# Optimization experiments

Measured on AMD Instinct MI355X. Metric: run time of the kernel, lower is better.

## Reference

```python
import jax, jax.numpy as jnp
import numpy as np

# Model hyperparameters (hardcoded in GarNetClassificationModel.__init__)
N_BLOCKS, N_AGG, N_FILT, N_PROP = 11, 4, 32, 20
B, V, F_IN = 128, 1024, 10
D_GEX = 2 * F_IN                                   # after GlobalExchange concat
D_UPD = N_FILT + N_AGG * 2 * (N_PROP + N_AGG) + N_AGG  # 32 + 192 + 4 = 228
BN_EPS = 1e-3                                      # keras BatchNormalization default


def setup_inputs() -> dict:
    key = jax.random.key(0)
    ks = iter(jax.random.split(key, 32))
    n = lambda shape, s=0.1: jax.random.normal(next(ks), shape, jnp.float32) * s
    return dict(
        x=jax.random.normal(next(ks), (B, V, F_IN), jnp.float32),
        bn0_gamma=jnp.ones((D_GEX,), jnp.float32),
        bn0_beta=jnp.zeros((D_GEX,), jnp.float32),
        bn0_mean=n((D_GEX,)),
        bn0_var=jax.random.uniform(next(ks), (D_GEX,), jnp.float32, 0.5, 1.5),
        W_in=n((D_GEX, N_FILT), 0.3),
        b_in=jnp.zeros((N_FILT,), jnp.float32),
        W_flr=n((N_BLOCKS, N_FILT, N_PROP), 0.2),
        b_flr=jnp.zeros((N_BLOCKS, N_PROP), jnp.float32),
        W_s=n((N_BLOCKS, N_FILT, N_AGG), 0.2),
        b_s=jnp.zeros((N_BLOCKS, N_AGG), jnp.float32),
        W_out=n((N_BLOCKS, D_UPD, N_FILT), 0.1),
        b_out=jnp.zeros((N_BLOCKS, N_FILT), jnp.float32),
        bn_gamma=jnp.ones((N_BLOCKS, N_FILT), jnp.float32),
        bn_beta=jnp.zeros((N_BLOCKS, N_FILT), jnp.float32),
        bn_mean=n((N_BLOCKS, N_FILT)),
        bn_var=jax.random.uniform(next(ks), (N_BLOCKS, N_FILT), jnp.float32, 0.5, 1.5),
        W_o0=n((N_BLOCKS * N_FILT, 48), 0.1),
        b_o0=jnp.zeros((48,), jnp.float32),
        W_o1=n((48, 3), 0.2),
        b_o1=jnp.zeros((3,), jnp.float32),
    )


def _bn(x, g, b, m, v):
    # inference-mode BatchNormalization over last axis
    return (x - m) * (g * jax.lax.rsqrt(v + BN_EPS)) + b


def reference(x, bn0_gamma, bn0_beta, bn0_mean, bn0_var, W_in, b_in,
              W_flr, b_flr, W_s, b_s, W_out, b_out,
              bn_gamma, bn_beta, bn_mean, bn_var,
              W_o0, b_o0, W_o1, b_o1):
    # GlobalExchange: concat per-event mean over vertices to each vertex
    mean = jnp.mean(x, axis=1, keepdims=True)                   # (B,1,F)
    h = jnp.concatenate([x, jnp.broadcast_to(mean, x.shape)], axis=-1)  # (B,V,2F)
    h = _bn(h, bn0_gamma, bn0_beta, bn0_mean, bn0_var)
    h = jnp.tanh(h @ W_in + b_in)                               # (B,V,32)

    def block(h, p):
        Wf, bf, Ws, bs, Wo, bo, g, be, m, v = p
        f = h @ Wf + bf                                  # (B,V,P) propagate features
        d = h @ Ws + bs                                  # (B,V,A) aggregator distances
        w = jnp.exp(-jnp.abs(d))                         # (B,V,A) edge weights
        feat = jnp.concatenate([f, w], axis=-1)          # (B,V,P+A)
        wf = w[..., None] * feat[:, :, None, :]          # (B,V,A,P+A)
        agg = jnp.concatenate([wf.max(axis=1), wf.mean(axis=1)], axis=-1)  # (B,A,2(P+A))
        upd = (w[..., None] * agg[:, None, :, :]).reshape(h.shape[0], h.shape[1], -1)  # (B,V,A*2(P+A))
        out = jnp.tanh(jnp.concatenate([h, upd, w], axis=-1) @ Wo + bo)  # (B,V,32)
        out = _bn(out, g, be, m, v)
        return out, out

    params = (W_flr, b_flr, W_s, b_s, W_out, b_out, bn_gamma, bn_beta, bn_mean, bn_var)
    _, feats = jax.lax.scan(block, h, params)            # feats: (L,B,V,32)
    feats = jnp.moveaxis(feats, 0, 2).reshape(x.shape[0], x.shape[1], -1)  # (B,V,L*32)

    h = jax.nn.relu(feats @ W_o0 + b_o0)                 # (B,V,48)
    return jax.nn.relu(h @ W_o1 + b_o1)                  # (B,V,3)
```

## Files before the change

kernel.cpp:

```cpp
#include <hip/hip_runtime.h>
#include <math.h>

#define NBLK  11
#define NAGG  4
#define NFILT 32
#define NPROP 20
#define BB    128
#define VV    1024
#define HV    512
#define FIN   10
#define TPB   512
#define BN_EPS 1e-3f
#define SHS   40
#define SFS   536

#define WSF_MEAN 128
#define WSF_AGG  (WSF_MEAN + BB*2*FIN)
#define WSF_FRAG (WSF_AGG + (BB*2*2) * NAGG * 48)
#define NFRAG    (NBLK*7*64*8)

typedef _Float16 f16;
typedef f16   f16x8 __attribute__((ext_vector_type(8)));
typedef float f32x4 __attribute__((ext_vector_type(4)));

__device__ __forceinline__ f32x4 MFMA(f16x8 a, f16x8 b, f32x4 c){
  return __builtin_amdgcn_mfma_f32_16x16x32_f16(a, b, c, 0, 0, 0);
}

__device__ __forceinline__ float fast_tanh(float x){
  float a = fabsf(x);
  float e = __expf(-2.0f * a);
  float r = (1.0f - e) / (1.0f + e);
  return copysignf(r, x);
}

extern "C" __global__ void garnet_prep(
    const float* __restrict__ W_flr, const float* __restrict__ W_s,
    const float* __restrict__ W_out, const float* __restrict__ W_o0,
    f16* __restrict__ frag)
{
  const int idx = blockIdx.x * blockDim.x + threadIdx.x;
  if (idx >= NFRAG) return;
  const int j    = idx & 7;
  const int lane = (idx >> 3) & 63;
  const int rest = idx >> 9;
  const int set  = rest % 7;
  const int l    = rest / 7;
  const int l16  = lane & 15, kb = lane >> 4, k = kb*8 + j;
  float val = 0.f;
  if (set < 2){
    const int n = set*16 + l16;
    if (set == 0) val = W_flr[l*NFILT*NPROP + k*NPROP + n];
    else          val = (n < 20) ? W_flr[l*NFILT*NPROP + k*NPROP + n]
                       : (n < 24 ? W_s[l*NFILT*NAGG + k*NAGG + (n-20)] : 0.f);
  } else if (set < 4){
    const int s = set - 2;
    val = W_out[l*228*NFILT + k*NFILT + s*16 + l16];
  } else {
    const int s = set - 4;
    val = W_o0[((size_t)l*NFILT + k)*48 + s*16 + l16];
  }
  frag[idx] = (f16)val;
}

extern "C" __global__ __launch_bounds__(TPB)
void garnet_fused(
    const float* __restrict__ x,
    const float* __restrict__ bn0_g, const float* __restrict__ bn0_b,
    const float* __restrict__ bn0_m, const float* __restrict__ bn0_v,
    const float* __restrict__ W_in,  const float* __restrict__ b_in,
    const float* __restrict__ W_flr, const float* __restrict__ b_flr,
    const float* __restrict__ W_s,   const float* __restrict__ b_s,
    const float* __restrict__ W_out, const float* __restrict__ b_out,
    const float* __restrict__ bn_g,  const float* __restrict__ bn_b,
    const float* __restrict__ bn_m,  const float* __restrict__ bn_v,
    const float* __restrict__ W_o0,  const float* __restrict__ b_o0,
    const float* __restrict__ W_o1,  const float* __restrict__ b_o1,
    int* __restrict__ wsFlag, float* __restrict__ wsF,
    const f16* __restrict__ frag,
    float* __restrict__ out)
{
  const int wg   = blockIdx.x;
  const int b    = wg & (BB - 1);
  const int half = wg >> 7;
  const int t    = threadIdx.x;
  const int lane = t & 63;
  const int wave = t >> 6;
  const int v    = half * HV + t;
  const int l16  = lane & 15;
  const int kb   = lane >> 4;

  __shared__ float sFeatT[24 * SFS];
  __shared__ __align__(16) f16 sHhi[HV * SHS];
  __shared__ __align__(16) f16 sHlo[HV * SHS];
  __shared__ f16   sMh[4 * 32];
  __shared__ float sAgg[NAGG][48];
  __shared__ float sRed[8][FIN];
  __shared__ float sMean[FIN];

  int* flag = wsFlag + b;

  f32x4 acc[4][3];

  auto phaseC = [&](int lc){
    f16x8 b3f[3];
    if (frag){
      const f16* flC = frag + (size_t)lc * 7 * 64 * 8;
      #pragma unroll
      for (int s = 0; s < 3; ++s)
        b3f[s] = *(const f16x8*)&flC[(size_t)((4 + s)*64 + lane)*8];
    } else {
      const float* Wo0l = W_o0 + (size_t)lc * NFILT * 48;
      #pragma unroll
      for (int s = 0; s < 3; ++s)
        #pragma unroll
        for (int j = 0; j < 8; ++j)
          b3f[s][j] = (f16)Wo0l[(kb*8 + j)*48 + s*16 + l16];
    }
    #pragma unroll
    for (int i = 0; i < 4; ++i){
      const int tb = wave*64 + i*16;
      const f16x8 ahi = *(const f16x8*)&sHhi[(tb + l16)*SHS + kb*8];
      const f16x8 alo = *(const f16x8*)&sHlo[(tb + l16)*SHS + kb*8];
      #pragma unroll
      for (int s = 0; s < 3; ++s){
        acc[i][s] = MFMA(ahi, b3f[s], acc[i][s]);
        acc[i][s] = MFMA(alo, b3f[s], acc[i][s]);
      }
    }
  };

  {
    float h[NFILT];
    float xv[FIN];
    const float* xp = x + ((size_t)b * VV + v) * FIN;
    #pragma unroll
    for (int c = 0; c < FIN; ++c) xv[c] = xp[c];

    float ps[FIN];
    #pragma unroll
    for (int c = 0; c < FIN; ++c) ps[c] = xv[c];
    #pragma unroll
    for (int m = 32; m > 0; m >>= 1){
      #pragma unroll
      for (int c = 0; c < FIN; ++c) ps[c] += __shfl_xor(ps[c], m, 64);
    }
    if (lane == 0){
      #pragma unroll
      for (int c = 0; c < FIN; ++c) sRed[wave][c] = ps[c];
    }
    __syncthreads();
    if (t < FIN){
      float s = 0.f;
      #pragma unroll
      for (int wv = 0; wv < 8; ++wv) s += sRed[wv][t];
      sRed[0][t] = s;
      __hip_atomic_store(&wsF[WSF_MEAN + (b*2 + half)*FIN + t], s,
                         __ATOMIC_RELAXED, __HIP_MEMORY_SCOPE_AGENT);
    }
    __syncthreads();
    if (t == 0){
      asm volatile("s_waitcnt vmcnt(0)" ::: "memory");
      __hip_atomic_fetch_add(flag, 1, __ATOMIC_RELAXED, __HIP_MEMORY_SCOPE_AGENT);
      while (__hip_atomic_load(flag, __ATOMIC_RELAXED, __HIP_MEMORY_SCOPE_AGENT) < 2)
        __builtin_amdgcn_s_sleep(2);
    }
    __syncthreads();
    if (t < FIN){
      float theirs = __hip_atomic_load(&wsF[WSF_MEAN + (b*2 + (half^1))*FIN + t],
                                       __ATOMIC_RELAXED, __HIP_MEMORY_SCOPE_AGENT);
      sMean[t] = (sRed[0][t] + theirs) * (1.0f / VV);
    }
    __syncthreads();

    float o[NFILT];
    #pragma unroll
    for (int j = 0; j < NFILT; ++j) o[j] = b_in[j];
    #pragma unroll
    for (int c = 0; c < FIN; ++c){
      const float zx = (xv[c]    - bn0_m[c])     * (bn0_g[c]     * rsqrtf(bn0_v[c]     + BN_EPS)) + bn0_b[c];
      const float zm = (sMean[c] - bn0_m[FIN+c]) * (bn0_g[FIN+c] * rsqrtf(bn0_v[FIN+c] + BN_EPS)) + bn0_b[FIN+c];
      #pragma unroll
      for (int j = 0; j < NFILT; ++j)
        o[j] += zx * W_in[c*NFILT + j] + zm * W_in[(FIN+c)*NFILT + j];
    }
    #pragma unroll
    for (int j = 0; j < NFILT; ++j) h[j] = fast_tanh(o[j]);

    #pragma unroll
    for (int c = 0; c < 4; ++c){
      f16x8 hh, hl;
      #pragma unroll
      for (int j = 0; j < 8; ++j){
        const float hv = h[c*8 + j];
        const f16 a = (f16)hv;
        hh[j] = a;
        hl[j] = (f16)(hv - (float)a);
      }
      *(f16x8*)&sHhi[t*SHS + c*8] = hh;
      *(f16x8*)&sHlo[t*SHS + c*8] = hl;
    }
  }
  __syncthreads();

  #pragma unroll
  for (int s = 0; s < 3; ++s){
    const float a0 = b_o0[s*16 + l16];
    #pragma unroll
    for (int i = 0; i < 4; ++i) acc[i][s] = (f32x4){a0, a0, a0, a0};
  }

  for (int l = 0; l < NBLK; ++l){
    const float* Wf = W_flr + l * NFILT * NPROP;
    const float* bf = b_flr + l * NPROP;
    const float* Ws = W_s   + l * NFILT * NAGG;
    const float* bs = b_s   + l * NAGG;
    const float* Wo = W_out + l * 228 * NFILT;
    const float* bo = b_out + l * NFILT;
    const float* g_ = bn_g  + l * NFILT;
    const float* be = bn_b  + l * NFILT;
    const float* bm = bn_m  + l * NFILT;
    const float* bv = bn_v  + l * NFILT;
    const f16*  fl  = frag + (size_t)l * 7 * 64 * 8;

    {
      f16x8 b1f0, b1f1;
      if (frag){
        b1f0 = *(const f16x8*)&fl[(size_t)(0*64 + lane)*8];
        b1f1 = *(const f16x8*)&fl[(size_t)(1*64 + lane)*8];
      } else {
        #pragma unroll
        for (int j = 0; j < 8; ++j){
          const int k = kb*8 + j;
          b1f0[j] = (f16)Wf[k*NPROP + l16];
          const int n = 16 + l16;
          b1f1[j] = (f16)((n < 20) ? Wf[k*NPROP + n] : (n < 24 ? Ws[k*NAGG + (n-20)] : 0.f));
        }
      }
      const float bias0 = bf[l16];
      const int  c1 = 16 + l16;
      const float bias1 = (c1 < 20) ? bf[c1] : (c1 < 24 ? bs[c1-20] : 0.f);

      #pragma unroll
      for (int i = 0; i < 4; ++i){
        const int tb = wave*64 + i*16;
        const f16x8 ahi = *(const f16x8*)&sHhi[(tb + l16)*SHS + kb*8];
        const f16x8 alo = *(const f16x8*)&sHlo[(tb + l16)*SHS + kb*8];
        f32x4 c0 = (f32x4){bias0, bias0, bias0, bias0};
        c0 = MFMA(ahi, b1f0, c0);
        c0 = MFMA(alo, b1f0, c0);
        *(f32x4*)&sFeatT[l16*SFS + tb + kb*4] = c0;
        f32x4 c1v = (f32x4){bias1, bias1, bias1, bias1};
        c1v = MFMA(ahi, b1f1, c1v);
        c1v = MFMA(alo, b1f1, c1v);
        if (l16 < 4){
          *(f32x4*)&sFeatT[(16 + l16)*SFS + tb + kb*4] = c1v;
        } else if (l16 < 8){
          f32x4 e;
          #pragma unroll
          for (int q = 0; q < 4; ++q) e[q] = __expf(-fabsf(c1v[q]));
          *(f32x4*)&sFeatT[(16 + l16)*SFS + tb + kb*4] = e;
        }
      }
    }
    __syncthreads();

    {
      const int w3 = wave * 3;
      float psum[NAGG][3], pmax[NAGG][3];
      #pragma unroll
      for (int a = 0; a < NAGG; ++a)
        #pragma unroll
        for (int c = 0; c < 3; ++c){ psum[a][c] = 0.f; pmax[a][c] = -INFINITY; }
      for (int i = 0; i < 8; ++i){
        const int row = i * 64 + lane;
        float fc[3], wa[NAGG];
        #pragma unroll
        for (int c = 0; c < 3; ++c) fc[c] = sFeatT[(w3 + c)*SFS + row];
        #pragma unroll
        for (int a = 0; a < NAGG; ++a) wa[a] = sFeatT[(20 + a)*SFS + row];
        #pragma unroll
        for (int a = 0; a < NAGG; ++a)
          #pragma unroll
          for (int c = 0; c < 3; ++c){
            const float p = wa[a] * fc[c];
            psum[a][c] += p;
            pmax[a][c]  = fmaxf(pmax[a][c], p);
          }
      }
      #pragma unroll
      for (int m = 32; m > 0; m >>= 1){
        #pragma unroll
        for (int a = 0; a < NAGG; ++a)
          #pragma unroll
          for (int c = 0; c < 3; ++c){
            psum[a][c] += __shfl_xor(psum[a][c], m, 64);
            pmax[a][c]  = fmaxf(pmax[a][c], __shfl_xor(pmax[a][c], m, 64));
          }
      }
      if (lane == 0){
        float* gp = wsF + WSF_AGG + (((size_t)(b*2 + (l&1))*2 + half) * NAGG * 48);
        #pragma unroll
        for (int a = 0; a < NAGG; ++a)
          #pragma unroll
          for (int c = 0; c < 3; ++c){
            sAgg[a][w3 + c]      = pmax[a][c];
            sAgg[a][24 + w3 + c] = psum[a][c];
            __hip_atomic_store(&gp[a*48 + w3 + c],      pmax[a][c], __ATOMIC_RELAXED, __HIP_MEMORY_SCOPE_AGENT);
            __hip_atomic_store(&gp[a*48 + 24 + w3 + c], psum[a][c], __ATOMIC_RELAXED, __HIP_MEMORY_SCOPE_AGENT);
          }
      }
    }
    __syncthreads();

    if (t == 0){
      asm volatile("s_waitcnt vmcnt(0)" ::: "memory");
      __hip_atomic_fetch_add(flag, 1, __ATOMIC_RELAXED, __HIP_MEMORY_SCOPE_AGENT);
    }
    __builtin_amdgcn_sched_barrier(0);
    if (l > 0) phaseC(l - 1);
    if (t == 0){
      while (__hip_atomic_load(flag, __ATOMIC_RELAXED, __HIP_MEMORY_SCOPE_AGENT) < 2*l + 4)
        __builtin_amdgcn_s_sleep(2);
    }
    __syncthreads();

    if (t < 192){
      const int a = t / 48, c = t - a * 48;
      const float* pp = wsF + WSF_AGG + (((size_t)(b*2 + (l&1))*2 + (half^1)) * NAGG * 48);
      const float mine   = sAgg[a][c];
      const float theirs = __hip_atomic_load(&pp[a*48 + c], __ATOMIC_RELAXED, __HIP_MEMORY_SCOPE_AGENT);
      sAgg[a][c] = (c < 24) ? fmaxf(mine, theirs) : (mine + theirs) * (1.0f / VV);
    }
    __syncthreads();

    if (t < 128){
      const int a = t >> 5, j = t & 31;
      float m = Wo[(224 + a) * NFILT + j];
      #pragma unroll 8
      for (int c = 0; c < 48; ++c) m += sAgg[a][c] * Wo[(32 + a*48 + c) * NFILT + j];
      sMh[a*32 + j] = (f16)m;
    }
    __syncthreads();

    {
      f16x8 b2f0, b2f1;
      if (frag){
        b2f0 = *(const f16x8*)&fl[(size_t)(2*64 + lane)*8];
        b2f1 = *(const f16x8*)&fl[(size_t)(3*64 + lane)*8];
      } else {
        #pragma unroll
        for (int j = 0; j < 8; ++j){
          const int k = kb*8 + j;
          b2f0[j] = (f16)Wo[k*NFILT + l16];
          b2f1[j] = (f16)Wo[k*NFILT + 16 + l16];
        }
      }
      f16x8 bmf[2];
      #pragma unroll
      for (int s = 0; s < 2; ++s)
        #pragma unroll
        for (int j = 0; j < 8; ++j)
          bmf[s][j] = (kb == 0 && j < 4) ? sMh[j*32 + s*16 + l16] : (f16)0.f;

      float boc[2], bmc[2], scc[2], bec[2];
      #pragma unroll
      for (int s = 0; s < 2; ++s){
        const int cc = s*16 + l16;
        boc[s] = bo[cc];
        bmc[s] = bm[cc];
        scc[s] = g_[cc] * rsqrtf(bv[cc] + BN_EPS);
        bec[s] = be[cc];
      }

      #pragma unroll
      for (int i = 0; i < 4; ++i){
        const int tb = wave*64 + i*16;
        const f16x8 ahi = *(const f16x8*)&sHhi[(tb + l16)*SHS + kb*8];
        const f16x8 alo = *(const f16x8*)&sHlo[(tb + l16)*SHS + kb*8];
        f16x8 wa;
        #pragma unroll
        for (int j = 0; j < 8; ++j) wa[j] = (f16)0.f;
        {
          const float w0 = sFeatT[20*SFS + tb + l16];
          const float w1 = sFeatT[21*SFS + tb + l16];
          const float w2 = sFeatT[22*SFS + tb + l16];
          const float w3v = sFeatT[23*SFS + tb + l16];
          if (kb == 0){ wa[0]=(f16)w0; wa[1]=(f16)w1; wa[2]=(f16)w2; wa[3]=(f16)w3v; }
        }
        #pragma unroll
        for (int s = 0; s < 2; ++s){
          f32x4 o = (f32x4){0.f, 0.f, 0.f, 0.f};
          o = MFMA(ahi, (s ? b2f1 : b2f0), o);
          o = MFMA(alo, (s ? b2f1 : b2f0), o);
          o = MFMA(wa,  bmf[s], o);
          #pragma unroll
          for (int q = 0; q < 4; ++q){
            const float th = fast_tanh(o[q] + boc[s]);
            const float hn = (th - bmc[s]) * scc[s] + bec[s];
            const f16 hh = (f16)hn;
            const int idx = (tb + kb*4 + q)*SHS + s*16 + l16;
            sHhi[idx] = hh;
            sHlo[idx] = (f16)(hn - (float)hh);
          }
        }
      }
    }
    asm volatile("s_waitcnt lgkmcnt(0)" ::: "memory");
  }

  phaseC(NBLK - 1);

  {
    float w1c[3][3];
    #pragma unroll
    for (int s = 0; s < 3; ++s)
      #pragma unroll
      for (int m = 0; m < 3; ++m) w1c[s][m] = W_o1[(s*16 + l16)*3 + m];
    const float bo1_0 = b_o1[0], bo1_1 = b_o1[1], bo1_2 = b_o1[2];

    #pragma unroll
    for (int i = 0; i < 4; ++i){
      const int tb = wave*64 + i*16;
      float p[4][3];
      #pragma unroll
      for (int q = 0; q < 4; ++q){ p[q][0]=0.f; p[q][1]=0.f; p[q][2]=0.f; }
      #pragma unroll
      for (int s = 0; s < 3; ++s)
        #pragma unroll
        for (int q = 0; q < 4; ++q){
          const float r_ = fmaxf(acc[i][s][q], 0.f);
          p[q][0] += r_ * w1c[s][0];
          p[q][1] += r_ * w1c[s][1];
          p[q][2] += r_ * w1c[s][2];
        }
      #pragma unroll
      for (int m = 1; m <= 8; m <<= 1)
        #pragma unroll
        for (int q = 0; q < 4; ++q){
          p[q][0] += __shfl_xor(p[q][0], m, 64);
          p[q][1] += __shfl_xor(p[q][1], m, 64);
          p[q][2] += __shfl_xor(p[q][2], m, 64);
        }
      if (l16 < 3){
        const float bo1v = (l16 == 0) ? bo1_0 : ((l16 == 1) ? bo1_1 : bo1_2);
        #pragma unroll
        for (int q = 0; q < 4; ++q){
          const float vv = (l16 == 0) ? p[q][0] : ((l16 == 1) ? p[q][1] : p[q][2]);
          out[((size_t)b*VV + half*HV + tb + kb*4 + q)*3 + l16] = fmaxf(vv + bo1v, 0.f);
        }
      }
    }
  }
}

extern "C" void kernel_launch(void* const* d_in, const int* in_sizes, int n_in,
                              void* d_out, int out_size, void* d_ws, size_t ws_size,
                              hipStream_t stream) {
  const float* x      = (const float*)d_in[0];
  const float* bn0_g  = (const float*)d_in[1];
  const float* bn0_b  = (const float*)d_in[2];
  const float* bn0_m  = (const float*)d_in[3];
  const float* bn0_v  = (const float*)d_in[4];
  const float* W_in   = (const float*)d_in[5];
  const float* b_in   = (const float*)d_in[6];
  const float* W_flr  = (const float*)d_in[7];
  const float* b_flr  = (const float*)d_in[8];
  const float* W_s    = (const float*)d_in[9];
  const float* b_s    = (const float*)d_in[10];
  const float* W_out  = (const float*)d_in[11];
  const float* b_out  = (const float*)d_in[12];
  const float* bn_g   = (const float*)d_in[13];
  const float* bn_b   = (const float*)d_in[14];
  const float* bn_m   = (const float*)d_in[15];
  const float* bn_v   = (const float*)d_in[16];
  const float* W_o0   = (const float*)d_in[17];
  const float* b_o0   = (const float*)d_in[18];
  const float* W_o1   = (const float*)d_in[19];
  const float* b_o1   = (const float*)d_in[20];

  float* wsF = (float*)d_ws;
  const size_t needed = (size_t)WSF_FRAG * 4 + (size_t)NFRAG * 2;
  _Float16* frag = (ws_size >= needed) ? (_Float16*)(wsF + WSF_FRAG) : nullptr;

  hipMemsetAsync(d_ws, 0, BB * sizeof(int), stream);

  if (frag)
    garnet_prep<<<dim3((NFRAG + 255) / 256), dim3(256), 0, stream>>>(
        W_flr, W_s, W_out, W_o0, frag);

  garnet_fused<<<dim3(BB * 2), dim3(TPB), 0, stream>>>(
      x, bn0_g, bn0_b, bn0_m, bn0_v, W_in, b_in,
      W_flr, b_flr, W_s, b_s, W_out, b_out,
      bn_g, bn_b, bn_m, bn_v, W_o0, b_o0, W_o1, b_o1,
      (int*)d_ws, wsF, frag, (float*)d_out);
}
```

Baseline: 164.7 us.

## Drop split-f16 hi/lo activations and store features in f16 with separate weight buffer

Removes the hi/lo f16 split of the hidden state, so each MFMA stage issues a single f16 multiply instead of two, and the low-part computation and stores go away. Propagated features are stored to LDS as f16 in a transposed buffer, and the exp edge weights go into a separate per-vertex float4 array, so they can be read with one vector load. This halves the MFMA work and reduces LDS footprint and traffic, which may raise occupancy. The cost is lower numerical precision of activations and features across 11 chained blocks.

New measurement: 164.0 us, median of 2. Within noise of the previous version (-0.4%).

```diff
diff --git a/kernel.cpp b/kernel.cpp
--- a/kernel.cpp
+++ b/kernel.cpp
@@ -12,7 +12,7 @@
 #define TPB   512
 #define BN_EPS 1e-3f
 #define SHS   40
-#define SFS   536
+#define SFTS  520
 
 #define WSF_MEAN 128
 #define WSF_AGG  (WSF_MEAN + BB*2*FIN)
@@ -20,6 +20,7 @@
 #define NFRAG    (NBLK*7*64*8)
 
 typedef _Float16 f16;
+typedef f16   f16x4 __attribute__((ext_vector_type(4)));
 typedef f16   f16x8 __attribute__((ext_vector_type(8)));
 typedef float f32x4 __attribute__((ext_vector_type(4)));
 
@@ -90,9 +91,9 @@
   const int l16  = lane & 15;
   const int kb   = lane >> 4;
 
-  __shared__ float sFeatT[24 * SFS];
-  __shared__ __align__(16) f16 sHhi[HV * SHS];
-  __shared__ __align__(16) f16 sHlo[HV * SHS];
+  __shared__ __align__(16) f16 sH[HV * SHS];
+  __shared__ __align__(16) f16 sFT[20 * SFTS];
+  __shared__ __align__(16) float sW[HV * 4];
   __shared__ f16   sMh[4 * 32];
   __shared__ float sAgg[NAGG][48];
   __shared__ float sRed[8][FIN];
@@ -120,13 +121,10 @@
     #pragma unroll
     for (int i = 0; i < 4; ++i){
       const int tb = wave*64 + i*16;
-      const f16x8 ahi = *(const f16x8*)&sHhi[(tb + l16)*SHS + kb*8];
-      const f16x8 alo = *(const f16x8*)&sHlo[(tb + l16)*SHS + kb*8];
-      #pragma unroll
-      for (int s = 0; s < 3; ++s){
-        acc[i][s] = MFMA(ahi, b3f[s], acc[i][s]);
-        acc[i][s] = MFMA(alo, b3f[s], acc[i][s]);
-      }
+      const f16x8 a_ = *(const f16x8*)&sH[(tb + l16)*SHS + kb*8];
+      #pragma unroll
+      for (int s = 0; s < 3; ++s)
+        acc[i][s] = MFMA(a_, b3f[s], acc[i][s]);
     }
   };
 
@@ -189,16 +187,10 @@
 
     #pragma unroll
     for (int c = 0; c < 4; ++c){
-      f16x8 hh, hl;
-      #pragma unroll
-      for (int j = 0; j < 8; ++j){
-        const float hv = h[c*8 + j];
-        const f16 a = (f16)hv;
-        hh[j] = a;
-        hl[j] = (f16)(hv - (float)a);
-      }
-      *(f16x8*)&sHhi[t*SHS + c*8] = hh;
-      *(f16x8*)&sHlo[t*SHS + c*8] = hl;
+      f16x8 hh;
+      #pragma unroll
+      for (int j = 0; j < 8; ++j) hh[j] = (f16)h[c*8 + j];
+      *(f16x8*)&sH[t*SHS + c*8] = hh;
     }
   }
   __syncthreads();
@@ -244,22 +236,25 @@
       #pragma unroll
       for (int i = 0; i < 4; ++i){
         const int tb = wave*64 + i*16;
-        const f16x8 ahi = *(const f16x8*)&sHhi[(tb + l16)*SHS + kb*8];
-        const f16x8 alo = *(const f16x8*)&sHlo[(tb + l16)*SHS + kb*8];
+        const f16x8 a_ = *(const f16x8*)&sH[(tb + l16)*SHS + kb*8];
         f32x4 c0 = (f32x4){bias0, bias0, bias0, bias0};
-        c0 = MFMA(ahi, b1f0, c0);
-        c0 = MFMA(alo, b1f0, c0);
-        *(f32x4*)&sFeatT[l16*SFS + tb + kb*4] = c0;
+        c0 = MFMA(a_, b1f0, c0);
+        f16x4 s0;
+        #pragma unroll
+        for (int q = 0; q < 4; ++q) s0[q] = (f16)c0[q];
+        *(f16x4*)&sFT[l16*SFTS + tb + kb*4] = s0;
+
         f32x4 c1v = (f32x4){bias1, bias1, bias1, bias1};
-        c1v = MFMA(ahi, b1f1, c1v);
-        c1v = MFMA(alo, b1f1, c1v);
+        c1v = MFMA(a_, b1f1, c1v);
         if (l16 < 4){
-          *(f32x4*)&sFeatT[(16 + l16)*SFS + tb + kb*4] = c1v;
+          f16x4 s1;
+          #pragma unroll
+          for (int q = 0; q < 4; ++q) s1[q] = (f16)c1v[q];
+          *(f16x4*)&sFT[(16 + l16)*SFTS + tb + kb*4] = s1;
         } else if (l16 < 8){
-          f32x4 e;
-          #pragma unroll
-          for (int q = 0; q < 4; ++q) e[q] = __expf(-fabsf(c1v[q]));
-          *(f32x4*)&sFeatT[(16 + l16)*SFS + tb + kb*4] = e;
+          #pragma unroll
+          for (int q = 0; q < 4; ++q)
+            sW[(tb + kb*4 + q)*4 + (l16 - 4)] = __expf(-fabsf(c1v[q]));
         }
       }
     }
@@ -274,16 +269,18 @@
         for (int c = 0; c < 3; ++c){ psum[a][c] = 0.f; pmax[a][c] = -INFINITY; }
       for (int i = 0; i < 8; ++i){
         const int row = i * 64 + lane;
-        float fc[3], wa[NAGG];
-        #pragma unroll
-        for (int c = 0; c < 3; ++c) fc[c] = sFeatT[(w3 + c)*SFS + row];
-        #pragma unroll
-        for (int a = 0; a < NAGG; ++a) wa[a] = sFeatT[(20 + a)*SFS + row];
+        const f32x4 wv = *(const f32x4*)&sW[row*4];
+        float fc[3];
+        #pragma unroll
+        for (int c = 0; c < 3; ++c){
+          const int col = w3 + c;
+          fc[c] = (col < 20) ? (float)sFT[col*SFTS + row] : wv[col - 20];
+        }
         #pragma unroll
         for (int a = 0; a < NAGG; ++a)
           #pragma unroll
           for (int c = 0; c < 3; ++c){
-            const float p = wa[a] * fc[c];
+            const float p = wv[a] * fc[c];
             psum[a][c] += p;
             pmax[a][c]  = fmaxf(pmax[a][c], p);
           }
@@ -376,32 +373,27 @@
       #pragma unroll
       for (int i = 0; i < 4; ++i){
         const int tb = wave*64 + i*16;
-        const f16x8 ahi = *(const f16x8*)&sHhi[(tb + l16)*SHS + kb*8];
-        const f16x8 alo = *(const f16x8*)&sHlo[(tb + l16)*SHS + kb*8];
+        const f16x8 a_ = *(const f16x8*)&sH[(tb + l16)*SHS + kb*8];
         f16x8 wa;
         #pragma unroll
         for (int j = 0; j < 8; ++j) wa[j] = (f16)0.f;
         {
-          const float w0 = sFeatT[20*SFS + tb + l16];
-          const float w1 = sFeatT[21*SFS + tb + l16];
-          const float w2 = sFeatT[22*SFS + tb + l16];
-          const float w3v = sFeatT[23*SFS + tb + l16];
-          if (kb == 0){ wa[0]=(f16)w0; wa[1]=(f16)w1; wa[2]=(f16)w2; wa[3]=(f16)w3v; }
+          const f32x4 wv = *(const f32x4*)&sW[(tb + l16)*4];
+          if (kb == 0){
+            wa[0] = (f16)wv[0]; wa[1] = (f16)wv[1];
+            wa[2] = (f16)wv[2]; wa[3] = (f16)wv[3];
+          }
         }
         #pragma unroll
         for (int s = 0; s < 2; ++s){
           f32x4 o = (f32x4){0.f, 0.f, 0.f, 0.f};
-          o = MFMA(ahi, (s ? b2f1 : b2f0), o);
-          o = MFMA(alo, (s ? b2f1 : b2f0), o);
-          o = MFMA(wa,  bmf[s], o);
+          o = MFMA(a_, (s ? b2f1 : b2f0), o);
+          o = MFMA(wa, bmf[s], o);
           #pragma unroll
           for (int q = 0; q < 4; ++q){
             const float th = fast_tanh(o[q] + boc[s]);
             const float hn = (th - bmc[s]) * scc[s] + bec[s];
-            const f16 hh = (f16)hn;
-            const int idx = (tb + kb*4 + q)*SHS + s*16 + l16;
-            sHhi[idx] = hh;
-            sHlo[idx] = (f16)(hn - (float)hh);
+            sH[(tb + kb*4 + q)*SHS + s*16 + l16] = (f16)hn;
           }
         }
       }
```

## Split each event across four vertex parts with two independent groups per workgroup

Applied to the files above, without the earlier changes.

Each event is now handled by four 256-vertex parts instead of two 512-vertex halves. Each 512-thread workgroup holds two independent 4-wave groups that serve different (event, part) pairs and synchronise with a custom LDS-atomic group barrier instead of __syncthreads. Per-layer features are stored in LDS as fp16 with a separate fp32 edge-weight array, which shrinks shared memory. The cross-part all-reduce of aggregates now combines four partial results through global memory, so there are more inter-workgroup flag spins and more reduction traffic in exchange for finer decoupling between groups.

After: 202.2 us. +22.8%, slower.

```diff
diff --git a/kernel.cpp b/kernel.cpp
--- a/kernel.cpp
+++ b/kernel.cpp
@@ -7,19 +7,21 @@
 #define NPROP 20
 #define BB    128
 #define VV    1024
-#define HV    512
+#define PARTS 4
+#define PV    256
 #define FIN   10
 #define TPB   512
 #define BN_EPS 1e-3f
 #define SHS   40
-#define SFS   536
+#define SFTS  264
 
 #define WSF_MEAN 128
-#define WSF_AGG  (WSF_MEAN + BB*2*FIN)
-#define WSF_FRAG (WSF_AGG + (BB*2*2) * NAGG * 48)
+#define WSF_AGG  (WSF_MEAN + BB*PARTS*FIN)
+#define WSF_END  (WSF_AGG + (BB*2) * PARTS * NAGG * 48)
 #define NFRAG    (NBLK*7*64*8)
 
 typedef _Float16 f16;
+typedef f16   f16x4 __attribute__((ext_vector_type(4)));
 typedef f16   f16x8 __attribute__((ext_vector_type(8)));
 typedef float f32x4 __attribute__((ext_vector_type(4)));
 
@@ -81,24 +83,43 @@
     float* __restrict__ out)
 {
   const int wg   = blockIdx.x;
-  const int b    = wg & (BB - 1);
-  const int half = wg >> 7;
   const int t    = threadIdx.x;
   const int lane = t & 63;
   const int wave = t >> 6;
-  const int v    = half * HV + t;
+  const int grp  = wave >> 2;
+  const int wv   = wave & 3;
+  const int tl   = t & 255;
+  const int gid  = wg * 2 + grp;
+  const int b    = gid & (BB - 1);
+  const int part = gid >> 7;
   const int l16  = lane & 15;
   const int kb   = lane >> 4;
 
-  __shared__ float sFeatT[24 * SFS];
-  __shared__ __align__(16) f16 sHhi[HV * SHS];
-  __shared__ __align__(16) f16 sHlo[HV * SHS];
-  __shared__ f16   sMh[4 * 32];
-  __shared__ float sAgg[NAGG][48];
-  __shared__ float sRed[8][FIN];
-  __shared__ float sMean[FIN];
+  __shared__ __align__(16) f16 sHhi[2][PV * SHS];
+  __shared__ __align__(16) f16 sHlo[2][PV * SHS];
+  __shared__ __align__(16) f16 sFT[2][20 * SFTS];
+  __shared__ __align__(16) float sW[2][PV * 4];
+  __shared__ f16   sMh[2][4 * 32];
+  __shared__ float sAgg[2][NAGG][48];
+  __shared__ float sRed[2][4][FIN];
+  __shared__ float sMean[2][FIN];
+  __shared__ int   gcnt[2];
 
   int* flag = wsFlag + b;
+  int gbt = 0;
+
+  auto grpbar = [&](){
+    gbt += 4;
+    asm volatile("s_waitcnt vmcnt(0) lgkmcnt(0)" ::: "memory");
+    if (lane == 0)
+      __hip_atomic_fetch_add(&gcnt[grp], 1, __ATOMIC_RELAXED, __HIP_MEMORY_SCOPE_WORKGROUP);
+    while (__hip_atomic_load(&gcnt[grp], __ATOMIC_RELAXED, __HIP_MEMORY_SCOPE_WORKGROUP) < gbt)
+      __builtin_amdgcn_s_sleep(1);
+    asm volatile("" ::: "memory");
+  };
+
+  if (t < 2) gcnt[t] = 0;
+  __syncthreads();
 
   f32x4 acc[4][3];
 
@@ -119,9 +140,9 @@
     }
     #pragma unroll
     for (int i = 0; i < 4; ++i){
-      const int tb = wave*64 + i*16;
-      const f16x8 ahi = *(const f16x8*)&sHhi[(tb + l16)*SHS + kb*8];
-      const f16x8 alo = *(const f16x8*)&sHlo[(tb + l16)*SHS + kb*8];
+      const int tb = wv*64 + i*16;
+      const f16x8 ahi = *(const f16x8*)&sHhi[grp][(tb + l16)*SHS + kb*8];
+      const f16x8 alo = *(const f16x8*)&sHlo[grp][(tb + l16)*SHS + kb*8];
       #pragma unroll
       for (int s = 0; s < 3; ++s){
         acc[i][s] = MFMA(ahi, b3f[s], acc[i][s]);
@@ -131,9 +152,8 @@
   };
 
   {
-    float h[NFILT];
     float xv[FIN];
-    const float* xp = x + ((size_t)b * VV + v) * FIN;
+    const float* xp = x + ((size_t)b * VV + part * PV + tl) * FIN;
     #pragma unroll
     for (int c = 0; c < FIN; ++c) xv[c] = xp[c];
 
@@ -147,61 +167,59 @@
     }
     if (lane == 0){
       #pragma unroll
-      for (int c = 0; c < FIN; ++c) sRed[wave][c] = ps[c];
-    }
-    __syncthreads();
-    if (t < FIN){
+      for (int c = 0; c < FIN; ++c) sRed[grp][wv][c] = ps[c];
+    }
+    grpbar();
+    if (tl < FIN){
       float s = 0.f;
       #pragma unroll
-      for (int wv = 0; wv < 8; ++wv) s += sRed[wv][t];
-      sRed[0][t] = s;
-      __hip_atomic_store(&wsF[WSF_MEAN + (b*2 + half)*FIN + t], s,
+      for (int w_ = 0; w_ < 4; ++w_) s += sRed[grp][w_][tl];
+      __hip_atomic_store(&wsF[WSF_MEAN + (b*PARTS + part)*FIN + tl], s,
                          __ATOMIC_RELAXED, __HIP_MEMORY_SCOPE_AGENT);
     }
-    __syncthreads();
-    if (t == 0){
-      asm volatile("s_waitcnt vmcnt(0)" ::: "memory");
+    grpbar();
+    if (tl == 0){
       __hip_atomic_fetch_add(flag, 1, __ATOMIC_RELAXED, __HIP_MEMORY_SCOPE_AGENT);
-      while (__hip_atomic_load(flag, __ATOMIC_RELAXED, __HIP_MEMORY_SCOPE_AGENT) < 2)
+      while (__hip_atomic_load(flag, __ATOMIC_RELAXED, __HIP_MEMORY_SCOPE_AGENT) < PARTS)
         __builtin_amdgcn_s_sleep(2);
     }
-    __syncthreads();
-    if (t < FIN){
-      float theirs = __hip_atomic_load(&wsF[WSF_MEAN + (b*2 + (half^1))*FIN + t],
-                                       __ATOMIC_RELAXED, __HIP_MEMORY_SCOPE_AGENT);
-      sMean[t] = (sRed[0][t] + theirs) * (1.0f / VV);
-    }
-    __syncthreads();
+    grpbar();
+    if (tl < FIN){
+      float s = 0.f;
+      #pragma unroll
+      for (int p = 0; p < PARTS; ++p)
+        s += __hip_atomic_load(&wsF[WSF_MEAN + (b*PARTS + p)*FIN + tl],
+                               __ATOMIC_RELAXED, __HIP_MEMORY_SCOPE_AGENT);
+      sMean[grp][tl] = s * (1.0f / VV);
+    }
+    grpbar();
 
     float o[NFILT];
     #pragma unroll
     for (int j = 0; j < NFILT; ++j) o[j] = b_in[j];
     #pragma unroll
     for (int c = 0; c < FIN; ++c){
-      const float zx = (xv[c]    - bn0_m[c])     * (bn0_g[c]     * rsqrtf(bn0_v[c]     + BN_EPS)) + bn0_b[c];
-      const float zm = (sMean[c] - bn0_m[FIN+c]) * (bn0_g[FIN+c] * rsqrtf(bn0_v[FIN+c] + BN_EPS)) + bn0_b[FIN+c];
+      const float zx = (xv[c]         - bn0_m[c])     * (bn0_g[c]     * rsqrtf(bn0_v[c]     + BN_EPS)) + bn0_b[c];
+      const float zm = (sMean[grp][c] - bn0_m[FIN+c]) * (bn0_g[FIN+c] * rsqrtf(bn0_v[FIN+c] + BN_EPS)) + bn0_b[FIN+c];
       #pragma unroll
       for (int j = 0; j < NFILT; ++j)
         o[j] += zx * W_in[c*NFILT + j] + zm * W_in[(FIN+c)*NFILT + j];
     }
     #pragma unroll
-    for (int j = 0; j < NFILT; ++j) h[j] = fast_tanh(o[j]);
-
-    #pragma unroll
-    for (int c = 0; c < 4; ++c){
+    for (int cc = 0; cc < 4; ++cc){
       f16x8 hh, hl;
       #pragma unroll
       for (int j = 0; j < 8; ++j){
-        const float hv = h[c*8 + j];
+        const float hv = fast_tanh(o[cc*8 + j]);
         const f16 a = (f16)hv;
         hh[j] = a;
         hl[j] = (f16)(hv - (float)a);
       }
-      *(f16x8*)&sHhi[t*SHS + c*8] = hh;
-      *(f16x8*)&sHlo[t*SHS + c*8] = hl;
-    }
+      *(f16x8*)&sHhi[grp][tl*SHS + cc*8] = hh;
+      *(f16x8*)&sHlo[grp][tl*SHS + cc*8] = hl;
+    }
+    grpbar();
   }
-  __syncthreads();
 
   #pragma unroll
   for (int s = 0; s < 3; ++s){
@@ -243,47 +261,57 @@
 
       #pragma unroll
       for (int i = 0; i < 4; ++i){
-        const int tb = wave*64 + i*16;
-        const f16x8 ahi = *(const f16x8*)&sHhi[(tb + l16)*SHS + kb*8];
-        const f16x8 alo = *(const f16x8*)&sHlo[(tb + l16)*SHS + kb*8];
+        const int tb = wv*64 + i*16;
+        const f16x8 ahi = *(const f16x8*)&sHhi[grp][(tb + l16)*SHS + kb*8];
+        const f16x8 alo = *(const f16x8*)&sHlo[grp][(tb + l16)*SHS + kb*8];
         f32x4 c0 = (f32x4){bias0, bias0, bias0, bias0};
         c0 = MFMA(ahi, b1f0, c0);
         c0 = MFMA(alo, b1f0, c0);
-        *(f32x4*)&sFeatT[l16*SFS + tb + kb*4] = c0;
+        f16x4 s0;
+        #pragma unroll
+        for (int q = 0; q < 4; ++q) s0[q] = (f16)c0[q];
+        *(f16x4*)&sFT[grp][l16*SFTS + tb + kb*4] = s0;
+
         f32x4 c1v = (f32x4){bias1, bias1, bias1, bias1};
         c1v = MFMA(ahi, b1f1, c1v);
         c1v = MFMA(alo, b1f1, c1v);
         if (l16 < 4){
-          *(f32x4*)&sFeatT[(16 + l16)*SFS + tb + kb*4] = c1v;
+          f16x4 s1;
+          #pragma unroll
+          for (int q = 0; q < 4; ++q) s1[q] = (f16)c1v[q];
+          *(f16x4*)&sFT[grp][(16 + l16)*SFTS + tb + kb*4] = s1;
         } else if (l16 < 8){
-          f32x4 e;
           #pragma unroll
-          for (int q = 0; q < 4; ++q) e[q] = __expf(-fabsf(c1v[q]));
-          *(f32x4*)&sFeatT[(16 + l16)*SFS + tb + kb*4] = e;
-        }
-      }
-    }
-    __syncthreads();
-
-    {
-      const int w3 = wave * 3;
+          for (int q = 0; q < 4; ++q)
+            sW[grp][(tb + kb*4 + q)*4 + (l16 - 4)] = __expf(-fabsf(c1v[q]));
+        }
+      }
+    }
+    grpbar();
+
+    #pragma unroll
+    for (int pass = 0; pass < 2; ++pass){
+      const int w3 = wv * 6 + pass * 3;
       float psum[NAGG][3], pmax[NAGG][3];
       #pragma unroll
       for (int a = 0; a < NAGG; ++a)
         #pragma unroll
         for (int c = 0; c < 3; ++c){ psum[a][c] = 0.f; pmax[a][c] = -INFINITY; }
-      for (int i = 0; i < 8; ++i){
+      #pragma unroll
+      for (int i = 0; i < 4; ++i){
         const int row = i * 64 + lane;
-        float fc[3], wa[NAGG];
-        #pragma unroll
-        for (int c = 0; c < 3; ++c) fc[c] = sFeatT[(w3 + c)*SFS + row];
-        #pragma unroll
-        for (int a = 0; a < NAGG; ++a) wa[a] = sFeatT[(20 + a)*SFS + row];
+        const f32x4 wvv = *(const f32x4*)&sW[grp][row*4];
+        float fc[3];
+        #pragma unroll
+        for (int c = 0; c < 3; ++c){
+          const int col = w3 + c;
+          fc[c] = (col < 20) ? (float)sFT[grp][col*SFTS + row] : wvv[col - 20];
+        }
         #pragma unroll
         for (int a = 0; a < NAGG; ++a)
           #pragma unroll
           for (int c = 0; c < 3; ++c){
-            const float p = wa[a] * fc[c];
+            const float p = wvv[a] * fc[c];
             psum[a][c] += p;
             pmax[a][c]  = fmaxf(pmax[a][c], p);
           }
@@ -299,49 +327,50 @@
           }
       }
       if (lane == 0){
-        float* gp = wsF + WSF_AGG + (((size_t)(b*2 + (l&1))*2 + half) * NAGG * 48);
+        float* gp = wsF + WSF_AGG + (((size_t)(b*2 + (l&1))*PARTS + part) * NAGG * 48);
         #pragma unroll
         for (int a = 0; a < NAGG; ++a)
           #pragma unroll
           for (int c = 0; c < 3; ++c){
-            sAgg[a][w3 + c]      = pmax[a][c];
-            sAgg[a][24 + w3 + c] = psum[a][c];
+            sAgg[grp][a][w3 + c]      = pmax[a][c];
+            sAgg[grp][a][24 + w3 + c] = psum[a][c];
             __hip_atomic_store(&gp[a*48 + w3 + c],      pmax[a][c], __ATOMIC_RELAXED, __HIP_MEMORY_SCOPE_AGENT);
             __hip_atomic_store(&gp[a*48 + 24 + w3 + c], psum[a][c], __ATOMIC_RELAXED, __HIP_MEMORY_SCOPE_AGENT);
           }
       }
     }
-    __syncthreads();
-
-    if (t == 0){
-      asm volatile("s_waitcnt vmcnt(0)" ::: "memory");
+    grpbar();
+
+    if (tl == 0)
       __hip_atomic_fetch_add(flag, 1, __ATOMIC_RELAXED, __HIP_MEMORY_SCOPE_AGENT);
-    }
     __builtin_amdgcn_sched_barrier(0);
     if (l > 0) phaseC(l - 1);
-    if (t == 0){
-      while (__hip_atomic_load(flag, __ATOMIC_RELAXED, __HIP_MEMORY_SCOPE_AGENT) < 2*l + 4)
+    if (tl == 0){
+      while (__hip_atomic_load(flag, __ATOMIC_RELAXED, __HIP_MEMORY_SCOPE_AGENT) < 4*l + 8)
         __builtin_amdgcn_s_sleep(2);
     }
-    __syncthreads();
-
-    if (t < 192){
-      const int a = t / 48, c = t - a * 48;
-      const float* pp = wsF + WSF_AGG + (((size_t)(b*2 + (l&1))*2 + (half^1)) * NAGG * 48);
-      const float mine   = sAgg[a][c];
-      const float theirs = __hip_atomic_load(&pp[a*48 + c], __ATOMIC_RELAXED, __HIP_MEMORY_SCOPE_AGENT);
-      sAgg[a][c] = (c < 24) ? fmaxf(mine, theirs) : (mine + theirs) * (1.0f / VV);
-    }
-    __syncthreads();
-
-    if (t < 128){
-      const int a = t >> 5, j = t & 31;
+    grpbar();
+
+    if (tl < 192){
+      const int a = tl / 48, c = tl - a * 48;
+      const size_t base = WSF_AGG + ((size_t)(b*2 + (l&1))*PARTS) * NAGG * 48;
+      float v0 = __hip_atomic_load(&wsF[base + (size_t)(0*NAGG*48) + a*48 + c], __ATOMIC_RELAXED, __HIP_MEMORY_SCOPE_AGENT);
+      float v1 = __hip_atomic_load(&wsF[base + (size_t)(1*NAGG*48) + a*48 + c], __ATOMIC_RELAXED, __HIP_MEMORY_SCOPE_AGENT);
+      float v2 = __hip_atomic_load(&wsF[base + (size_t)(2*NAGG*48) + a*48 + c], __ATOMIC_RELAXED, __HIP_MEMORY_SCOPE_AGENT);
+      float v3 = __hip_atomic_load(&wsF[base + (size_t)(3*NAGG*48) + a*48 + c], __ATOMIC_RELAXED, __HIP_MEMORY_SCOPE_AGENT);
+      sAgg[grp][a][c] = (c < 24) ? fmaxf(fmaxf(v0, v1), fmaxf(v2, v3))
+                                 : (v0 + v1 + v2 + v3) * (1.0f / VV);
+    }
+    grpbar();
+
+    if (tl < 128){
+      const int a = tl >> 5, j = tl & 31;
       float m = Wo[(224 + a) * NFILT + j];
       #pragma unroll 8
-      for (int c = 0; c < 48; ++c) m += sAgg[a][c] * Wo[(32 + a*48 + c) * NFILT + j];
-      sMh[a*32 + j] = (f16)m;
-    }
-    __syncthreads();
+      for (int c = 0; c < 48; ++c) m += sAgg[grp][a][c] * Wo[(32 + a*48 + c) * NFILT + j];
+      sMh[grp][a*32 + j] = (f16)m;
+    }
+    grpbar();
 
     {
       f16x8 b2f0, b2f1;
@@ -361,7 +390,7 @@
       for (int s = 0; s < 2; ++s)
         #pragma unroll
         for (int j = 0; j < 8; ++j)
-          bmf[s][j] = (kb == 0 && j < 4) ? sMh[j*32 + s*16 + l16] : (f16)0.f;
+          bmf[s][j] = (kb == 0 && j < 4) ? sMh[grp][j*32 + s*16 + l16] : (f16)0.f;
 
       float boc[2], bmc[2], scc[2], bec[2];
       #pragma unroll
@@ -375,18 +404,18 @@
 
       #pragma unroll
       for (int i = 0; i < 4; ++i){
-        const int tb = wave*64 + i*16;
-        const f16x8 ahi = *(const f16x8*)&sHhi[(tb + l16)*SHS + kb*8];
-        const f16x8 alo = *(const f16x8*)&sHlo[(tb + l16)*SHS + kb*8];
+        const int tb = wv*64 + i*16;
+        const f16x8 ahi = *(const f16x8*)&sHhi[grp][(tb + l16)*SHS + kb*8];
+        const f16x8 alo = *(const f16x8*)&sHlo[grp][(tb + l16)*SHS + kb*8];
         f16x8 wa;
         #pragma unroll
         for (int j = 0; j < 8; ++j) wa[j] = (f16)0.f;
         {
-          const float w0 = sFeatT[20*SFS + tb + l16];
-          const float w1 = sFeatT[21*SFS + tb + l16];
-          const float w2 = sFeatT[22*SFS + tb + l16];
-          const float w3v = sFeatT[23*SFS + tb + l16];
-          if (kb == 0){ wa[0]=(f16)w0; wa[1]=(f16)w1; wa[2]=(f16)w2; wa[3]=(f16)w3v; }
+          const f32x4 wvv = *(const f32x4*)&sW[grp][(tb + l16)*4];
+          if (kb == 0){
+            wa[0] = (f16)wvv[0]; wa[1] = (f16)wvv[1];
+            wa[2] = (f16)wvv[2]; wa[3] = (f16)wvv[3];
+          }
         }
         #pragma unroll
         for (int s = 0; s < 2; ++s){
@@ -400,8 +429,8 @@
             const float hn = (th - bmc[s]) * scc[s] + bec[s];
             const f16 hh = (f16)hn;
             const int idx = (tb + kb*4 + q)*SHS + s*16 + l16;
-            sHhi[idx] = hh;
-            sHlo[idx] = (f16)(hn - (float)hh);
+            sHhi[grp][idx] = hh;
+            sHlo[grp][idx] = (f16)(hn - (float)hh);
           }
         }
       }
@@ -421,7 +450,7 @@
 
     #pragma unroll
     for (int i = 0; i < 4; ++i){
-      const int tb = wave*64 + i*16;
+      const int tb = wv*64 + i*16;
       float p[4][3];
       #pragma unroll
       for (int q = 0; q < 4; ++q){ p[q][0]=0.f; p[q][1]=0.f; p[q][2]=0.f; }
@@ -447,7 +476,7 @@
         #pragma unroll
         for (int q = 0; q < 4; ++q){
           const float vv = (l16 == 0) ? p[q][0] : ((l16 == 1) ? p[q][1] : p[q][2]);
-          out[((size_t)b*VV + half*HV + tb + kb*4 + q)*3 + l16] = fmaxf(vv + bo1v, 0.f);
+          out[((size_t)b*VV + part*PV + tb + kb*4 + q)*3 + l16] = fmaxf(vv + bo1v, 0.f);
         }
       }
     }
@@ -480,8 +509,8 @@
   const float* b_o1   = (const float*)d_in[20];
 
   float* wsF = (float*)d_ws;
-  const size_t needed = (size_t)WSF_FRAG * 4 + (size_t)NFRAG * 2;
-  _Float16* frag = (ws_size >= needed) ? (_Float16*)(wsF + WSF_FRAG) : nullptr;
+  const size_t needed = (size_t)WSF_END * 4 + (size_t)NFRAG * 2;
+  _Float16* frag = (ws_size >= needed) ? (_Float16*)(wsF + WSF_END) : nullptr;
 
   hipMemsetAsync(d_ws, 0, BB * sizeof(int), stream);
 
```
